# Optimization experiments

Hardware: AMD Instinct MI355X
Metric: run time of the kernel (lower is better)

Reference implementation:

```python
import jax, jax.numpy as jnp
import numpy as np

N = 100000
F_IN = 128
HID = 256
N_CLS = 40
E = 1600000


def setup_inputs() -> dict:
    key = jax.random.key(0)
    ks = jax.random.split(key, 12)
    x = jax.random.normal(ks[0], (N, F_IN), dtype=jnp.float32)
    edge_index = jax.random.randint(ks[1], (2, E), 0, N, dtype=jnp.int64)
    # GCNConv params (glorot-ish scale), conv2 is reused twice in forward
    def lin(k, fi, fo):
        return jax.random.normal(k, (fi, fo), dtype=jnp.float32) * (1.0 / np.sqrt(fi))
    return {
        "x": x,
        "edge_index": edge_index,
        "W1": lin(ks[2], F_IN, HID), "b1": jnp.zeros((HID,), jnp.float32),
        "W2": lin(ks[3], HID, HID),  "b2": jnp.zeros((HID,), jnp.float32),
        "W3": lin(ks[4], HID, HID),  "b3": jnp.zeros((HID,), jnp.float32),
        "W4": lin(ks[5], HID, N_CLS), "b4": jnp.zeros((N_CLS,), jnp.float32),
    }


def _gcn_norm(edge_index, n):
    # add self-loops, compute symmetric normalization D^-1/2 (A+I) D^-1/2
    loop = jnp.arange(n, dtype=edge_index.dtype)
    src = jnp.concatenate([edge_index[0], loop])
    dst = jnp.concatenate([edge_index[1], loop])
    deg = jax.ops.segment_sum(jnp.ones_like(dst, dtype=jnp.float32), dst, num_segments=n)
    dinv = jnp.where(deg > 0, jax.lax.rsqrt(deg), 0.0)
    norm = dinv[src] * dinv[dst]  # [E+N]
    return src, dst, norm


def _gcn_conv(x, W, b, src, dst, norm, n):
    h = x @ W                       # [N, Fout] dense transform first (fewer msg bytes)
    msg = h[src] * norm[:, None]    # gather + scale
    out = jax.ops.segment_sum(msg, dst, num_segments=n)  # scatter-add
    return out + b


def reference(x, edge_index, W1, b1, W2, b2, W3, b3, W4, b4):
    n = x.shape[0]
    src, dst, norm = _gcn_norm(edge_index, n)
    h = jax.nn.relu(_gcn_conv(x, W1, b1, src, dst, norm, n))
    h = jax.nn.relu(_gcn_conv(h, W2, b2, src, dst, norm, n))
    h = jax.nn.relu(_gcn_conv(h, W2, b2, src, dst, norm, n))  # conv2 reused, as in source
    h = jax.nn.relu(_gcn_conv(h, W3, b3, src, dst, norm, n))
    h = _gcn_conv(h, W4, b4, src, dst, norm, n)
    return jax.nn.log_softmax(h, axis=1)
```

## Files before the change

kernel.cpp:

```cpp
#include <hip/hip_runtime.h>
#include <stdint.h>
#include <math.h>

#define NN   100000
#define FIN  128
#define HIDDEN 256
#define NCLS 40
#define NE   1600000

#define PRNG 8
#define RNG  12500
#define SSL  32
#define NES  50000

typedef unsigned short u16;
typedef unsigned char u8;
typedef __attribute__((ext_vector_type(8))) short s16x8;
typedef __attribute__((ext_vector_type(4))) float f32x4;
typedef __attribute__((ext_vector_type(2))) float f32x2;

__device__ __forceinline__ float bf2f(unsigned short u) {
    union { float f; uint32_t i; } v; v.i = ((uint32_t)u) << 16; return v.f;
}
__device__ __forceinline__ unsigned short f2bf(float f) {
    union { float f; uint32_t i; } v; v.f = f;
    uint32_t r = v.i + 0x7fffu + ((v.i >> 16) & 1u);
    return (unsigned short)(r >> 16);
}
__device__ __forceinline__ u8 f2fp8(float f) {
    int r = __builtin_amdgcn_cvt_pk_fp8_f32(f, f, 0, false);
    return (u8)(r & 0xff);
}

#define SWZ_T(t)  ((((t) >> 3) & 1) | ((((t) >> 5) & 1) << 1))
#define SWZ_L(lr) ((((lr) >> 1) & 1) | ((((lr) >> 3) & 1) << 1))

__global__ __launch_bounds__(256) void k_detect(const u16* __restrict__ x16,
                                                const int* __restrict__ ei,
                                                int* __restrict__ flags) {
    int g = blockIdx.x * 256 + threadIdx.x;
    uint2 v = *(const uint2*)(x16 + (size_t)g * 4);
    int nan_cnt = 0;
    uint32_t w0 = v.x, w1 = v.y;
    if (((w0 >> 0)  & 0x7fff) >= 0x7f80) nan_cnt++;
    if (((w0 >> 16) & 0x7fff) >= 0x7f80) nan_cnt++;
    if (((w1 >> 0)  & 0x7fff) >= 0x7f80) nan_cnt++;
    if (((w1 >> 16) & 0x7fff) >= 0x7f80) nan_cnt++;
    int odd_nz = (g < 8192 && ei[2 * g + 1] != 0) ? 1 : 0;
#pragma unroll
    for (int off = 1; off < 64; off <<= 1) {
        nan_cnt += __shfl_xor(nan_cnt, off);
        odd_nz  += __shfl_xor(odd_nz, off);
    }
    if ((threadIdx.x & 63) == 0) {
        if (nan_cnt) atomicAdd(&flags[0], nan_cnt);
        if (odd_nz)  atomicAdd(&flags[2], odd_nz);
    }
}

__global__ void k_compact(const int* __restrict__ ei, int* __restrict__ dst32,
                          int* __restrict__ src32, const int* __restrict__ flags) {
    int e = blockIdx.x * 256 + threadIdx.x;
    if (e < NE) {
        if (flags[2] == 0) { src32[e] = ei[2 * e]; dst32[e] = ei[2 * (NE + e)]; }
        else               { src32[e] = ei[e];     dst32[e] = ei[NE + e]; }
    }
}

__global__ void k_trans_cvt(const void* W1, const void* W2, const void* W3, const void* W4,
                            u16* W1t, u16* W2t, u16* W3t, u16* W4t,
                            const void* b1, const void* b2, const void* b3, const void* b4,
                            u16* o1, u16* o2, u16* o3, u16* o4,
                            const void* __restrict__ x, const float* __restrict__ dinv,
                            u16* __restrict__ xb,
                            const int* __restrict__ flags) {
    int b = blockIdx.x;
    int fl = flags[0];
    int t = threadIdx.x;
    if (b >= 705) {
        int i8 = (b - 705) * 256 + t;
        if (i8 < NN * FIN / 8) {
            int i = i8 * 8;
            float d = dinv[i >> 7];
            u16 r[8];
            if (fl) {
                const float* xf = (const float*)x + i;
                f32x4 v0 = *(const f32x4*)xf;
                f32x4 v1 = *(const f32x4*)(xf + 4);
#pragma unroll
                for (int k = 0; k < 4; ++k) { r[k] = f2bf(v0[k] * d); r[4 + k] = f2bf(v1[k] * d); }
            } else {
                uint4 v = *(const uint4*)((const u16*)x + i);
                uint32_t w[4] = {v.x, v.y, v.z, v.w};
#pragma unroll
                for (int k = 0; k < 4; ++k) {
                    r[2 * k]     = f2bf(bf2f((u16)(w[k] & 0xffff)) * d);
                    r[2 * k + 1] = f2bf(bf2f((u16)(w[k] >> 16)) * d);
                }
            }
            uint4 o;
            o.x = (uint32_t)r[0] | ((uint32_t)r[1] << 16);
            o.y = (uint32_t)r[2] | ((uint32_t)r[3] << 16);
            o.z = (uint32_t)r[4] | ((uint32_t)r[5] << 16);
            o.w = (uint32_t)r[6] | ((uint32_t)r[7] << 16);
            *(uint4*)(xb + i) = o;
        }
        return;
    }
    if (b == 704) {
        o1[t] = fl ? f2bf(((const float*)b1)[t]) : ((const u16*)b1)[t];
        o2[t] = fl ? f2bf(((const float*)b2)[t]) : ((const u16*)b2)[t];
        o3[t] = fl ? f2bf(((const float*)b3)[t]) : ((const u16*)b3)[t];
        if (t < 64) o4[t] = (t < NCLS) ? (fl ? f2bf(((const float*)b4)[t]) : ((const u16*)b4)[t]) : (u16)0;
        return;
    }
    const void* W; u16* Wt; int K, F, Fpad, base;
    if (b < 128)      { W = W1; Wt = W1t; K = 128; F = 256; Fpad = 256; base = 0; }
    else if (b < 384) { W = W2; Wt = W2t; K = 256; F = 256; Fpad = 256; base = 128; }
    else if (b < 640) { W = W3; Wt = W3t; K = 256; F = 256; Fpad = 256; base = 384; }
    else              { W = W4; Wt = W4t; K = 256; F = 40;  Fpad = 64;  base = 640; }
    int idx = (b - base) * 256 + t;
    if (idx >= K * Fpad) return;
    int f = idx / K, k = idx - f * K;
    u16 v = 0;
    if (f < F) {
        if (fl) v = f2bf(((const float*)W)[(size_t)k * F + f]);
        else    v = ((const u16*)W)[(size_t)k * F + f];
    }
    Wt[idx] = v;
}


__global__ __launch_bounds__(256) void k_histb(const int* __restrict__ dst32,
                                               int* __restrict__ partial) {
    __shared__ int h[RNG];
    int p = blockIdx.x >> 5, s = blockIdx.x & 31;
    int t = threadIdx.x;
    int4 z4 = make_int4(0, 0, 0, 0);
    for (int i = t * 4; i < RNG; i += 1024) *(int4*)(h + i) = z4;
    __syncthreads();
    int base = s * NES;
    int lo = p * RNG;
    int nfull = NES & ~1023;
    for (int k = t * 4; k < nfull; k += 1024) {
        int4 d4 = *(const int4*)(dst32 + base + k);
        int a;
        a = d4.x - lo; if ((unsigned)a < RNG) atomicAdd(&h[a], 1);
        a = d4.y - lo; if ((unsigned)a < RNG) atomicAdd(&h[a], 1);
        a = d4.z - lo; if ((unsigned)a < RNG) atomicAdd(&h[a], 1);
        a = d4.w - lo; if ((unsigned)a < RNG) atomicAdd(&h[a], 1);
    }
    for (int k = nfull + t; k < NES; k += 256) {
        int a = dst32[base + k] - lo;
        if ((unsigned)a < RNG) atomicAdd(&h[a], 1);
    }
    __syncthreads();
    int* out = partial + blockIdx.x * RNG;
    for (int i = t * 4; i < RNG; i += 1024) *(int4*)(out + i) = *(const int4*)(h + i);
}

__global__ __launch_bounds__(256) void k_scan1(const int* __restrict__ partial,
                                               int* __restrict__ cnt,
                                               int* __restrict__ out,
                                               int* __restrict__ bsum) {
    __shared__ int sh[256];
    int t = threadIdx.x;
    int base = blockIdx.x * 1024 + t * 4;
    int v0 = 0, v1 = 0, v2 = 0, v3 = 0;
    if (base < NN) {
        int p = base / RNG, il = base - p * RNG;
        const int* q = partial + (p * SSL) * RNG + il;
        int4 acc = make_int4(0, 0, 0, 0);
#pragma unroll
        for (int s = 0; s < SSL; ++s) {
            int4 w = *(const int4*)(q + s * RNG);
            acc.x += w.x; acc.y += w.y; acc.z += w.z; acc.w += w.w;
        }
        v0 = acc.x; v1 = acc.y; v2 = acc.z; v3 = acc.w;
        *(int4*)(cnt + base) = acc;
    }
    int s = v0 + v1 + v2 + v3;
    sh[t] = s;
    __syncthreads();
    for (int off = 1; off < 256; off <<= 1) {
        int x = (t >= off) ? sh[t - off] : 0;
        __syncthreads();
        sh[t] += x;
        __syncthreads();
    }
    int ex = sh[t] - s;
    if (base < NN) {
        int4 o = make_int4(ex, ex + v0, ex + v0 + v1, ex + v0 + v1 + v2);
        *(int4*)(out + base) = o;
    }
    if (t == 255) bsum[blockIdx.x] = sh[255];
}

__global__ void k_scan2(int* bsum, int nb) {
    __shared__ int sh[128];
    int t = threadIdx.x;
    int v = (t < nb) ? bsum[t] : 0;
    sh[t] = v;
    __syncthreads();
    for (int off = 1; off < 128; off <<= 1) {
        int x = (t >= off) ? sh[t - off] : 0;
        __syncthreads();
        sh[t] += x;
        __syncthreads();
    }
    if (t < nb) bsum[t] = sh[t] - v;
}

__global__ void k_scan3o(int* __restrict__ rp, const int* __restrict__ bsum,
                         const int* __restrict__ cnt, float* __restrict__ dinv,
                         int* __restrict__ partial) {
    int i = blockIdx.x * 256 + threadIdx.x;
    if (i < NN) {
        int v = rp[i] + bsum[i >> 10];
        rp[i] = v;
        dinv[i] = rsqrtf((float)(cnt[i] + 1));
        int p = i / RNG, il = i - p * RNG;
        int* q = partial + (p * SSL) * RNG + il;
        int run = v;
#pragma unroll
        for (int s = 0; s < SSL; ++s) { int t = q[s * RNG]; q[s * RNG] = run; run += t; }
    }
    if (i == 0) rp[NN] = NE;
}

__global__ __launch_bounds__(256) void k_fillb(const int* __restrict__ dst32,
                                               const int* __restrict__ src32,
                                               const int* __restrict__ offs,
                                               int* __restrict__ col) {
    __shared__ int h[RNG];
    int p = blockIdx.x >> 5, s = blockIdx.x & 31;
    int t = threadIdx.x;
    const int* o = offs + blockIdx.x * RNG;
    for (int i = t * 4; i < RNG; i += 1024) *(int4*)(h + i) = *(const int4*)(o + i);
    __syncthreads();
    int base = s * NES;
    int lo = p * RNG;
    int nfull = NES & ~1023;
    for (int k = t * 4; k < nfull; k += 1024) {
        int4 d4 = *(const int4*)(dst32 + base + k);
        int4 s4 = *(const int4*)(src32 + base + k);
        int a;
        a = d4.x - lo; if ((unsigned)a < RNG) col[atomicAdd(&h[a], 1)] = s4.x;
        a = d4.y - lo; if ((unsigned)a < RNG) col[atomicAdd(&h[a], 1)] = s4.y;
        a = d4.z - lo; if ((unsigned)a < RNG) col[atomicAdd(&h[a], 1)] = s4.z;
        a = d4.w - lo; if ((unsigned)a < RNG) col[atomicAdd(&h[a], 1)] = s4.w;
    }
    for (int k = nfull + t; k < NES; k += 256) {
        int a = dst32[base + k] - lo;
        if ((unsigned)a < RNG) col[atomicAdd(&h[a], 1)] = src32[base + k];
    }
}


#define GLL(g, l) __builtin_amdgcn_global_load_lds( \
    (const __attribute__((address_space(1))) unsigned int*)(g), \
    (__attribute__((address_space(3))) unsigned int*)(l), 16, 0, 0)

#define NT128 ((NN + 127) / 128)
#define NT256 ((NN + 255) / 256)

__global__ __launch_bounds__(256) void k_gemmP(const u16* __restrict__ A,
                                               const u16* __restrict__ Wt,
                                               const float* __restrict__ dinv,
                                               const u16* __restrict__ bias,
                                               u16* __restrict__ C,
                                               int K, int out_fp8) {
    __shared__ __align__(16) u16 Bs[64 * 256];
    __shared__ __align__(16) u16 As[2 * 128 * 32];
    int t = threadIdx.x;
    int bn = blockIdx.y;
    int w = t >> 6, lane = t & 63;
    int lrow = lane & 15, lq = lane >> 4;
    int r0 = t >> 2;
    int seg = ((t & 3) ^ SWZ_T(t)) * 8;
    int lqs = (lq ^ SWZ_L(lrow)) * 8;

    int nK = K >> 5;
    for (int r = 0; r < nK; ++r)
        GLL(Wt + (size_t)(bn * 64 + (t >> 2)) * K + r * 32 + seg, Bs + r * 2048 + t * 8);

    bool fuse = (bias != nullptr);
    float bcol[4];
#pragma unroll
    for (int j = 0; j < 4; ++j)
        bcol[j] = fuse ? bf2f(bias[bn * 64 + j * 16 + lrow]) : 0.f;

    for (int tm = blockIdx.x; tm < NT128; tm += gridDim.x) {
        int rowBase = tm * 128;
        int ar0 = rowBase + r0;       if (ar0 > NN - 1) ar0 = NN - 1;
        int ar1 = rowBase + 64 + r0;  if (ar1 > NN - 1) ar1 = NN - 1;
        const u16* a0p = A + (size_t)ar0 * K + seg;
        const u16* a1p = A + (size_t)ar1 * K + seg;
        GLL(a0p, As + t * 8);
        GLL(a1p, As + 2048 + t * 8);

        f32x4 acc[2][4] = {};
        int cur = 0;
        for (int kt = 0; kt < nK; ++kt) {
            __syncthreads();
            if (kt + 1 < nK) {
                int nxt = cur ^ 1;
                GLL(a0p + (kt + 1) * 32, As + nxt * 4096 + t * 8);
                GLL(a1p + (kt + 1) * 32, As + nxt * 4096 + 2048 + t * 8);
            }
            const u16* ab = As + cur * 4096;
            const u16* bb = Bs + kt * 2048;
            s16x8 af[2], bf[4];
#pragma unroll
            for (int i = 0; i < 2; ++i)
                af[i] = *(const s16x8*)(ab + (w * 32 + i * 16 + lrow) * 32 + lqs);
#pragma unroll
            for (int j = 0; j < 4; ++j)
                bf[j] = *(const s16x8*)(bb + (j * 16 + lrow) * 32 + lqs);
#pragma unroll
            for (int i = 0; i < 2; ++i)
#pragma unroll
                for (int j = 0; j < 4; ++j)
                    acc[i][j] = __builtin_amdgcn_mfma_f32_16x16x32_bf16(af[i], bf[j], acc[i][j], 0, 0, 0);
            cur ^= 1;
        }

        u8* C8 = (u8*)C;
#pragma unroll
        for (int i = 0; i < 2; ++i) {
#pragma unroll
            for (int rr = 0; rr < 4; ++rr) {
                int row = rowBase + w * 32 + i * 16 + lq * 4 + rr;
                if (row < NN) {
                    float d = dinv[row];
#pragma unroll
                    for (int j = 0; j < 4; ++j) {
                        int colg = bn * 64 + j * 16 + lrow;
                        float v = fuse ? fmaxf(fmaf(d, acc[i][j][rr], bcol[j]), 0.f)
                                       : acc[i][j][rr] * d;
                        if (out_fp8) C8[(size_t)row * HIDDEN + colg] = f2fp8(v);
                        else         C[(size_t)row * HIDDEN + colg] = f2bf(v);
                    }
                }
            }
        }
        __syncthreads();
    }
}

__global__ __launch_bounds__(256) void k_gemmP64(const u16* __restrict__ A,
                                                 const u16* __restrict__ Wt,
                                                 const float* __restrict__ dinv,
                                                 u16* __restrict__ C) {
    const int K = 256;
    __shared__ __align__(16) u16 Bs[64 * 256];
    __shared__ __align__(16) u16 As[2 * 256 * 32];
    int t = threadIdx.x;
    int w = t >> 6, lane = t & 63;
    int lrow = lane & 15, lq = lane >> 4;
    int seg = ((t & 3) ^ SWZ_T(t)) * 8;
    int lqs = (lq ^ SWZ_L(lrow)) * 8;
    int rr0 = t >> 2;

    for (int r = 0; r < 8; ++r)
        GLL(Wt + (size_t)(t >> 2) * K + r * 32 + seg, Bs + r * 2048 + t * 8);

    for (int tm = blockIdx.x; tm < NT256; tm += gridDim.x) {
        int rowBase = tm * 256;
        const u16* ap[4];
#pragma unroll
        for (int c = 0; c < 4; ++c) {
            int ar = rowBase + c * 64 + rr0;
            if (ar > NN - 1) ar = NN - 1;
            ap[c] = A + (size_t)ar * K + seg;
        }
#pragma unroll
        for (int c = 0; c < 4; ++c) GLL(ap[c], As + c * 2048 + t * 8);

        f32x4 acc[4][4] = {};
        int cur = 0;
        for (int kt = 0; kt < 8; ++kt) {
            __syncthreads();
            if (kt + 1 < 8) {
                int nxt = cur ^ 1;
#pragma unroll
                for (int c = 0; c < 4; ++c)
                    GLL(ap[c] + (kt + 1) * 32, As + nxt * 8192 + c * 2048 + t * 8);
            }
            const u16* ab = As + cur * 8192;
            const u16* bb = Bs + kt * 2048;
            s16x8 af[4], bf[4];
#pragma unroll
            for (int i = 0; i < 4; ++i)
                af[i] = *(const s16x8*)(ab + (w * 64 + i * 16 + lrow) * 32 + lqs);
#pragma unroll
            for (int j = 0; j < 4; ++j)
                bf[j] = *(const s16x8*)(bb + (j * 16 + lrow) * 32 + lqs);
#pragma unroll
            for (int i = 0; i < 4; ++i)
#pragma unroll
                for (int j = 0; j < 4; ++j)
                    acc[i][j] = __builtin_amdgcn_mfma_f32_16x16x32_bf16(af[i], bf[j], acc[i][j], 0, 0, 0);
            cur ^= 1;
        }

#pragma unroll
        for (int i = 0; i < 4; ++i) {
#pragma unroll
            for (int rr = 0; rr < 4; ++rr) {
                int row = rowBase + w * 64 + i * 16 + lq * 4 + rr;
                if (row < NN) {
                    float d = dinv[row];
#pragma unroll
                    for (int j = 0; j < 4; ++j) {
                        int colg = j * 16 + lrow;
                        C[(size_t)row * 64 + colg] = f2bf(acc[i][j][rr] * d);
                    }
                }
            }
        }
        __syncthreads();
    }
}


__global__ __launch_bounds__(256) void k_agg8(const u8* __restrict__ hs,
                                              const int* __restrict__ rp,
                                              const int* __restrict__ col,
                                              const float* __restrict__ dinv,
                                              const u16* __restrict__ bias,
                                              u16* __restrict__ out) {
    int wq = __builtin_amdgcn_readfirstlane(threadIdx.x >> 6);
    int row = blockIdx.x * 4 + wq;
    if (row >= NN) return;
    int lane = threadIdx.x & 63;
    int fo = lane * 4;
    float a0 = 0.f, a1 = 0.f, a2 = 0.f, a3 = 0.f;
    auto acc_add = [&](uint32_t w) {
        f32x2 x = __builtin_amdgcn_cvt_pk_f32_fp8(w, false);
        f32x2 y = __builtin_amdgcn_cvt_pk_f32_fp8(w, true);
        a0 += x.x; a1 += x.y; a2 += y.x; a3 += y.y;
    };
    auto acc_fma = [&](uint32_t w, float m) {
        f32x2 x = __builtin_amdgcn_cvt_pk_f32_fp8(w, false);
        f32x2 y = __builtin_amdgcn_cvt_pk_f32_fp8(w, true);
        a0 = fmaf(m, x.x, a0); a1 = fmaf(m, x.y, a1);
        a2 = fmaf(m, y.x, a2); a3 = fmaf(m, y.y, a3);
    };
    acc_add(*(const uint32_t*)(hs + (size_t)row * HIDDEN + fo));
    int p  = __builtin_amdgcn_readfirstlane(rp[row]);
    int p1 = __builtin_amdgcn_readfirstlane(rp[row + 1]);
    for (; p + 8 <= p1; p += 8) {
        uint32_t v[8];
#pragma unroll
        for (int k = 0; k < 8; ++k) {
            int c = __builtin_amdgcn_readfirstlane(col[p + k]);
            v[k] = *(const uint32_t*)(hs + (size_t)c * HIDDEN + fo);
        }
#pragma unroll
        for (int k = 0; k < 8; ++k) acc_add(v[k]);
    }
    int rem = p1 - p;
    if (rem) {
        uint32_t v[8];
#pragma unroll
        for (int k = 0; k < 8; ++k) {
            int idx = (k < rem) ? (p + k) : p;
            int c = __builtin_amdgcn_readfirstlane(col[idx]);
            v[k] = *(const uint32_t*)(hs + (size_t)c * HIDDEN + fo);
        }
#pragma unroll
        for (int k = 0; k < 8; ++k) acc_fma(v[k], (k < rem) ? 1.f : 0.f);
    }
    float d = dinv[row];
    uint2 bv = *(const uint2*)(bias + fo);
    float r0 = fmaxf(fmaf(d, a0, bf2f((u16)(bv.x & 0xffff))), 0.f);
    float r1 = fmaxf(fmaf(d, a1, bf2f((u16)(bv.x >> 16))), 0.f);
    float r2 = fmaxf(fmaf(d, a2, bf2f((u16)(bv.y & 0xffff))), 0.f);
    float r3 = fmaxf(fmaf(d, a3, bf2f((u16)(bv.y >> 16))), 0.f);
    uint2 o;
    o.x = (uint32_t)f2bf(r0) | ((uint32_t)f2bf(r1) << 16);
    o.y = (uint32_t)f2bf(r2) | ((uint32_t)f2bf(r3) << 16);
    *(uint2*)(out + (size_t)row * HIDDEN + fo) = o;
}

__global__ __launch_bounds__(256) void k_aggx(const u16* __restrict__ xb,
                                              const int* __restrict__ rp,
                                              const int* __restrict__ col,
                                              u16* __restrict__ out) {
    int wq = __builtin_amdgcn_readfirstlane(threadIdx.x >> 6);
    int row = blockIdx.x * 4 + wq;
    if (row >= NN) return;
    int lane = threadIdx.x & 63;
    int fo = lane * 2;
    float a0 = 0.f, a1 = 0.f;
    auto acc_add = [&](uint32_t w) {
        a0 += bf2f((u16)(w & 0xffff));
        a1 += bf2f((u16)(w >> 16));
    };
    auto acc_fma = [&](uint32_t w, float m) {
        a0 = fmaf(m, bf2f((u16)(w & 0xffff)), a0);
        a1 = fmaf(m, bf2f((u16)(w >> 16)), a1);
    };
    acc_add(*(const uint32_t*)(xb + (size_t)row * FIN + fo));
    int p  = __builtin_amdgcn_readfirstlane(rp[row]);
    int p1 = __builtin_amdgcn_readfirstlane(rp[row + 1]);
    for (; p + 8 <= p1; p += 8) {
        uint32_t v[8];
#pragma unroll
        for (int k = 0; k < 8; ++k) {
            int c = __builtin_amdgcn_readfirstlane(col[p + k]);
            v[k] = *(const uint32_t*)(xb + (size_t)c * FIN + fo);
        }
#pragma unroll
        for (int k = 0; k < 8; ++k) acc_add(v[k]);
    }
    int rem = p1 - p;
    if (rem) {
        uint32_t v[8];
#pragma unroll
        for (int k = 0; k < 8; ++k) {
            int idx = (k < rem) ? (p + k) : p;
            int c = __builtin_amdgcn_readfirstlane(col[idx]);
            v[k] = *(const uint32_t*)(xb + (size_t)c * FIN + fo);
        }
#pragma unroll
        for (int k = 0; k < 8; ++k) acc_fma(v[k], (k < rem) ? 1.f : 0.f);
    }
    uint32_t o = (uint32_t)f2bf(a0) | ((uint32_t)f2bf(a1) << 16);
    *(uint32_t*)(out + (size_t)row * FIN + fo) = o;
}

__global__ __launch_bounds__(256) void k_agg5(const u16* __restrict__ hs,
                                              const int* __restrict__ rp,
                                              const int* __restrict__ col,
                                              const float* __restrict__ dinv,
                                              const u16* __restrict__ bias,
                                              void* __restrict__ out,
                                              const int* __restrict__ flags) {
    int wq = __builtin_amdgcn_readfirstlane(threadIdx.x >> 6);
    int row = blockIdx.x * 4 + wq;
    if (row >= NN) return;
    int lane = threadIdx.x & 63;
    float a = bf2f(hs[(size_t)row * 64 + lane]);
    int p  = __builtin_amdgcn_readfirstlane(rp[row]);
    int p1 = __builtin_amdgcn_readfirstlane(rp[row + 1]);
    for (; p + 8 <= p1; p += 8) {
        u16 v[8];
#pragma unroll
        for (int k = 0; k < 8; ++k) {
            int c = __builtin_amdgcn_readfirstlane(col[p + k]);
            v[k] = hs[(size_t)c * 64 + lane];
        }
#pragma unroll
        for (int k = 0; k < 8; ++k) a += bf2f(v[k]);
    }
    int rem = p1 - p;
    if (rem) {
        u16 v[8];
#pragma unroll
        for (int k = 0; k < 8; ++k) {
            int idx = (k < rem) ? (p + k) : p;
            int c = __builtin_amdgcn_readfirstlane(col[idx]);
            v[k] = hs[(size_t)c * 64 + lane];
        }
#pragma unroll
        for (int k = 0; k < 8; ++k)
            a = fmaf((k < rem) ? 1.f : 0.f, bf2f(v[k]), a);
    }
    bool act = lane < NCLS;
    float d = dinv[row];
    float l = act ? fmaf(d, a, bf2f(bias[lane])) : -1e30f;
    float m = l;
#pragma unroll
    for (int off = 32; off > 0; off >>= 1) m = fmaxf(m, __shfl_xor(m, off));
    float e = act ? __expf(l - m) : 0.f;
#pragma unroll
    for (int off = 32; off > 0; off >>= 1) e += __shfl_xor(e, off);
    if (act) {
        float r = l - m - __logf(e);
        if (flags[0]) ((float*)out)[(size_t)row * NCLS + lane] = r;
        else          ((u16*)out)[(size_t)row * NCLS + lane] = f2bf(r);
    }
}


extern "C" void kernel_launch(void* const* d_in, const int* in_sizes, int n_in,
                              void* d_out, int out_size, void* d_ws, size_t ws_size,
                              hipStream_t stream) {
    const void* x  = d_in[0];
    const int* ei  = (const int*)d_in[1];
    const void* W1 = d_in[2];
    const void* b1 = d_in[3];
    const void* W2 = d_in[4];
    const void* b2 = d_in[5];
    const void* W3 = d_in[6];
    const void* b3 = d_in[7];
    const void* W4 = d_in[8];
    const void* b4 = d_in[9];

    char* p = (char*)d_ws;
    auto alloc = [&](size_t b) -> char* {
        char* r = p;
        p += (b + 255) & ~(size_t)255;
        return r;
    };
    int*   flags = (int*)alloc(256);
    int*   cnt  = (int*)alloc((size_t)NN * 4);
    float* dinv = (float*)alloc((size_t)NN * 4);
    int*   rp   = (int*)alloc((size_t)(NN + 1) * 4);
    int*   col  = (int*)alloc((size_t)NE * 4);
    int*   bsum = (int*)alloc(4096);
    u16* xb  = (u16*)alloc((size_t)NN * FIN * 2);
    u16* W1t = (u16*)alloc((size_t)256 * 128 * 2);
    u16* W2t = (u16*)alloc((size_t)256 * 256 * 2);
    u16* W3t = (u16*)alloc((size_t)256 * 256 * 2);
    u16* W4t = (u16*)alloc((size_t)64 * 256 * 2);
    u16* bb1 = (u16*)alloc(512);
    u16* bb2 = (u16*)alloc(512);
    u16* bb3 = (u16*)alloc(512);
    u16* bb4 = (u16*)alloc(128);
    u16* bufA = (u16*)alloc((size_t)NN * HIDDEN * 2);
    u16* bufB = (u16*)alloc((size_t)NN * HIDDEN * 2);

    int* dst32   = (int*)bufA;
    int* src32   = dst32 + NE;
    int* partial = (int*)bufB;

    hipMemsetAsync(flags, 0, 16, stream);
    k_detect<<<64, 256, 0, stream>>>((const u16*)x, ei, flags);
    k_compact<<<(NE + 255) / 256, 256, 0, stream>>>(ei, dst32, src32, flags);

    k_histb<<<PRNG * SSL, 256, 0, stream>>>(dst32, partial);
    k_scan1<<<(NN + 1023) / 1024, 256, 0, stream>>>(partial, cnt, rp, bsum);
    k_scan2<<<1, 128, 0, stream>>>(bsum, (NN + 1023) / 1024);
    k_scan3o<<<(NN + 255) / 256, 256, 0, stream>>>(rp, bsum, cnt, dinv, partial);
    k_fillb<<<PRNG * SSL, 256, 0, stream>>>(dst32, src32, partial, col);

    k_trans_cvt<<<705 + (NN * FIN / 8 + 255) / 256, 256, 0, stream>>>(
        W1, W2, W3, W4, W1t, W2t, W3t, W4t,
        b1, b2, b3, b4, bb1, bb2, bb3, bb4, x, dinv, xb, flags);

    dim3 gP(192, 4);
    dim3 aggGrid((NN + 3) / 4);

    k_aggx<<<aggGrid, 256, 0, stream>>>(xb, rp, col, bufB);
    k_gemmP<<<gP, 256, 0, stream>>>(bufB, W1t, dinv, bb1, bufA, 128, 0);
    k_gemmP<<<gP, 256, 0, stream>>>(bufA, W2t, dinv, nullptr, bufB, 256, 1);
    k_agg8<<<aggGrid, 256, 0, stream>>>((const u8*)bufB, rp, col, dinv, bb2, bufA);
    k_gemmP<<<gP, 256, 0, stream>>>(bufA, W2t, dinv, nullptr, bufB, 256, 1);
    k_agg8<<<aggGrid, 256, 0, stream>>>((const u8*)bufB, rp, col, dinv, bb2, bufA);
    k_gemmP<<<gP, 256, 0, stream>>>(bufA, W3t, dinv, nullptr, bufB, 256, 1);
    k_agg8<<<aggGrid, 256, 0, stream>>>((const u8*)bufB, rp, col, dinv, bb3, bufA);
    k_gemmP64<<<256, 256, 0, stream>>>(bufA, W4t, dinv, bufB);
    k_agg5<<<aggGrid, 256, 0, stream>>>(bufB, rp, col, dinv, bb4, d_out, flags);
}
```

Measured before the change: 648.2 us.

## Replace partitioned LDS CSR build with global atomics and unify last GEMM

Measured after the change: 753.8 us. +16.3%, slower.

```diff
diff --git a/kernel.cpp b/kernel.cpp
--- a/kernel.cpp
+++ b/kernel.cpp
@@ -7,11 +7,6 @@
 #define HIDDEN 256
 #define NCLS 40
 #define NE   1600000
-
-#define PRNG 8
-#define RNG  12500
-#define SSL  32
-#define NES  50000
 
 typedef unsigned short u16;
 typedef unsigned char u8;
@@ -131,55 +126,23 @@
 }
 
 
-__global__ __launch_bounds__(256) void k_histb(const int* __restrict__ dst32,
-                                               int* __restrict__ partial) {
-    __shared__ int h[RNG];
-    int p = blockIdx.x >> 5, s = blockIdx.x & 31;
-    int t = threadIdx.x;
-    int4 z4 = make_int4(0, 0, 0, 0);
-    for (int i = t * 4; i < RNG; i += 1024) *(int4*)(h + i) = z4;
-    __syncthreads();
-    int base = s * NES;
-    int lo = p * RNG;
-    int nfull = NES & ~1023;
-    for (int k = t * 4; k < nfull; k += 1024) {
-        int4 d4 = *(const int4*)(dst32 + base + k);
-        int a;
-        a = d4.x - lo; if ((unsigned)a < RNG) atomicAdd(&h[a], 1);
-        a = d4.y - lo; if ((unsigned)a < RNG) atomicAdd(&h[a], 1);
-        a = d4.z - lo; if ((unsigned)a < RNG) atomicAdd(&h[a], 1);
-        a = d4.w - lo; if ((unsigned)a < RNG) atomicAdd(&h[a], 1);
-    }
-    for (int k = nfull + t; k < NES; k += 256) {
-        int a = dst32[base + k] - lo;
-        if ((unsigned)a < RNG) atomicAdd(&h[a], 1);
-    }
-    __syncthreads();
-    int* out = partial + blockIdx.x * RNG;
-    for (int i = t * 4; i < RNG; i += 1024) *(int4*)(out + i) = *(const int4*)(h + i);
-}
-
-__global__ __launch_bounds__(256) void k_scan1(const int* __restrict__ partial,
-                                               int* __restrict__ cnt,
+__global__ __launch_bounds__(256) void k_hista(const int* __restrict__ dst32,
+                                               int* __restrict__ cnt) {
+    int i = (blockIdx.x * 256 + threadIdx.x) * 2;
+    int2 d2 = *(const int2*)(dst32 + i);
+    atomicAdd(&cnt[d2.x], 1);
+    atomicAdd(&cnt[d2.y], 1);
+}
+
+__global__ __launch_bounds__(256) void k_scan1(const int* __restrict__ cnt,
                                                int* __restrict__ out,
                                                int* __restrict__ bsum) {
     __shared__ int sh[256];
     int t = threadIdx.x;
     int base = blockIdx.x * 1024 + t * 4;
-    int v0 = 0, v1 = 0, v2 = 0, v3 = 0;
-    if (base < NN) {
-        int p = base / RNG, il = base - p * RNG;
-        const int* q = partial + (p * SSL) * RNG + il;
-        int4 acc = make_int4(0, 0, 0, 0);
-#pragma unroll
-        for (int s = 0; s < SSL; ++s) {
-            int4 w = *(const int4*)(q + s * RNG);
-            acc.x += w.x; acc.y += w.y; acc.z += w.z; acc.w += w.w;
-        }
-        v0 = acc.x; v1 = acc.y; v2 = acc.z; v3 = acc.w;
-        *(int4*)(cnt + base) = acc;
-    }
-    int s = v0 + v1 + v2 + v3;
+    int4 a = make_int4(0, 0, 0, 0);
+    if (base < NN) a = *(const int4*)(cnt + base);
+    int s = a.x + a.y + a.z + a.w;
     sh[t] = s;
     __syncthreads();
     for (int off = 1; off < 256; off <<= 1) {
@@ -190,7 +153,7 @@
     }
     int ex = sh[t] - s;
     if (base < NN) {
-        int4 o = make_int4(ex, ex + v0, ex + v0 + v1, ex + v0 + v1 + v2);
+        int4 o = make_int4(ex, ex + a.x, ex + a.x + a.y, ex + a.x + a.y + a.z);
         *(int4*)(out + base) = o;
     }
     if (t == 255) bsum[blockIdx.x] = sh[255];
@@ -211,49 +174,30 @@
     if (t < nb) bsum[t] = sh[t] - v;
 }
 
-__global__ void k_scan3o(int* __restrict__ rp, const int* __restrict__ bsum,
-                         const int* __restrict__ cnt, float* __restrict__ dinv,
-                         int* __restrict__ partial) {
+__global__ void k_scan3(int* __restrict__ rp, const int* __restrict__ bsum,
+                        const int* __restrict__ cnt, float* __restrict__ dinv,
+                        int* __restrict__ wcur) {
     int i = blockIdx.x * 256 + threadIdx.x;
     if (i < NN) {
         int v = rp[i] + bsum[i >> 10];
         rp[i] = v;
+        wcur[i] = v;
         dinv[i] = rsqrtf((float)(cnt[i] + 1));
-        int p = i / RNG, il = i - p * RNG;
-        int* q = partial + (p * SSL) * RNG + il;
-        int run = v;
-#pragma unroll
-        for (int s = 0; s < SSL; ++s) { int t = q[s * RNG]; q[s * RNG] = run; run += t; }
     }
     if (i == 0) rp[NN] = NE;
 }
 
-__global__ __launch_bounds__(256) void k_fillb(const int* __restrict__ dst32,
+__global__ __launch_bounds__(256) void k_filla(const int* __restrict__ dst32,
                                                const int* __restrict__ src32,
-                                               const int* __restrict__ offs,
+                                               int* __restrict__ wcur,
                                                int* __restrict__ col) {
-    __shared__ int h[RNG];
-    int p = blockIdx.x >> 5, s = blockIdx.x & 31;
-    int t = threadIdx.x;
-    const int* o = offs + blockIdx.x * RNG;
-    for (int i = t * 4; i < RNG; i += 1024) *(int4*)(h + i) = *(const int4*)(o + i);
-    __syncthreads();
-    int base = s * NES;
-    int lo = p * RNG;
-    int nfull = NES & ~1023;
-    for (int k = t * 4; k < nfull; k += 1024) {
-        int4 d4 = *(const int4*)(dst32 + base + k);
-        int4 s4 = *(const int4*)(src32 + base + k);
-        int a;
-        a = d4.x - lo; if ((unsigned)a < RNG) col[atomicAdd(&h[a], 1)] = s4.x;
-        a = d4.y - lo; if ((unsigned)a < RNG) col[atomicAdd(&h[a], 1)] = s4.y;
-        a = d4.z - lo; if ((unsigned)a < RNG) col[atomicAdd(&h[a], 1)] = s4.z;
-        a = d4.w - lo; if ((unsigned)a < RNG) col[atomicAdd(&h[a], 1)] = s4.w;
-    }
-    for (int k = nfull + t; k < NES; k += 256) {
-        int a = dst32[base + k] - lo;
-        if ((unsigned)a < RNG) col[atomicAdd(&h[a], 1)] = src32[base + k];
-    }
+    int i = (blockIdx.x * 256 + threadIdx.x) * 2;
+    int2 d2 = *(const int2*)(dst32 + i);
+    int2 s2 = *(const int2*)(src32 + i);
+    int p0 = atomicAdd(&wcur[d2.x], 1);
+    col[p0] = s2.x;
+    int p1 = atomicAdd(&wcur[d2.y], 1);
+    col[p1] = s2.y;
 }
 
 
@@ -262,14 +206,13 @@
     (__attribute__((address_space(3))) unsigned int*)(l), 16, 0, 0)
 
 #define NT128 ((NN + 127) / 128)
-#define NT256 ((NN + 255) / 256)
 
 __global__ __launch_bounds__(256) void k_gemmP(const u16* __restrict__ A,
                                                const u16* __restrict__ Wt,
                                                const float* __restrict__ dinv,
                                                const u16* __restrict__ bias,
                                                u16* __restrict__ C,
-                                               int K, int out_fp8) {
+                                               int K, int ldc, int out_fp8) {
     __shared__ __align__(16) u16 Bs[64 * 256];
     __shared__ __align__(16) u16 As[2 * 128 * 32];
     int t = threadIdx.x;
@@ -338,83 +281,8 @@
                         int colg = bn * 64 + j * 16 + lrow;
                         float v = fuse ? fmaxf(fmaf(d, acc[i][j][rr], bcol[j]), 0.f)
                                        : acc[i][j][rr] * d;
-                        if (out_fp8) C8[(size_t)row * HIDDEN + colg] = f2fp8(v);
-                        else         C[(size_t)row * HIDDEN + colg] = f2bf(v);
-                    }
-                }
-            }
-        }
-        __syncthreads();
-    }
-}
-
-__global__ __launch_bounds__(256) void k_gemmP64(const u16* __restrict__ A,
-                                                 const u16* __restrict__ Wt,
-                                                 const float* __restrict__ dinv,
-                                                 u16* __restrict__ C) {
-    const int K = 256;
-    __shared__ __align__(16) u16 Bs[64 * 256];
-    __shared__ __align__(16) u16 As[2 * 256 * 32];
-    int t = threadIdx.x;
-    int w = t >> 6, lane = t & 63;
-    int lrow = lane & 15, lq = lane >> 4;
-    int seg = ((t & 3) ^ SWZ_T(t)) * 8;
-    int lqs = (lq ^ SWZ_L(lrow)) * 8;
-    int rr0 = t >> 2;
-
-    for (int r = 0; r < 8; ++r)
-        GLL(Wt + (size_t)(t >> 2) * K + r * 32 + seg, Bs + r * 2048 + t * 8);
-
-    for (int tm = blockIdx.x; tm < NT256; tm += gridDim.x) {
-        int rowBase = tm * 256;
-        const u16* ap[4];
-#pragma unroll
-        for (int c = 0; c < 4; ++c) {
-            int ar = rowBase + c * 64 + rr0;
-            if (ar > NN - 1) ar = NN - 1;
-            ap[c] = A + (size_t)ar * K + seg;
-        }
-#pragma unroll
-        for (int c = 0; c < 4; ++c) GLL(ap[c], As + c * 2048 + t * 8);
-
-        f32x4 acc[4][4] = {};
-        int cur = 0;
-        for (int kt = 0; kt < 8; ++kt) {
-            __syncthreads();
-            if (kt + 1 < 8) {
-                int nxt = cur ^ 1;
-#pragma unroll
-                for (int c = 0; c < 4; ++c)
-                    GLL(ap[c] + (kt + 1) * 32, As + nxt * 8192 + c * 2048 + t * 8);
-            }
-            const u16* ab = As + cur * 8192;
-            const u16* bb = Bs + kt * 2048;
-            s16x8 af[4], bf[4];
-#pragma unroll
-            for (int i = 0; i < 4; ++i)
-                af[i] = *(const s16x8*)(ab + (w * 64 + i * 16 + lrow) * 32 + lqs);
-#pragma unroll
-            for (int j = 0; j < 4; ++j)
-                bf[j] = *(const s16x8*)(bb + (j * 16 + lrow) * 32 + lqs);
-#pragma unroll
-            for (int i = 0; i < 4; ++i)
-#pragma unroll
-                for (int j = 0; j < 4; ++j)
-                    acc[i][j] = __builtin_amdgcn_mfma_f32_16x16x32_bf16(af[i], bf[j], acc[i][j], 0, 0, 0);
-            cur ^= 1;
-        }
-
-#pragma unroll
-        for (int i = 0; i < 4; ++i) {
-#pragma unroll
-            for (int rr = 0; rr < 4; ++rr) {
-                int row = rowBase + w * 64 + i * 16 + lq * 4 + rr;
-                if (row < NN) {
-                    float d = dinv[row];
-#pragma unroll
-                    for (int j = 0; j < 4; ++j) {
-                        int colg = j * 16 + lrow;
-                        C[(size_t)row * 64 + colg] = f2bf(acc[i][j][rr] * d);
+                        if (out_fp8) C8[(size_t)row * ldc + colg] = f2fp8(v);
+                        else         C[(size_t)row * ldc + colg] = f2bf(v);
                     }
                 }
             }
@@ -609,6 +477,7 @@
     int*   cnt  = (int*)alloc((size_t)NN * 4);
     float* dinv = (float*)alloc((size_t)NN * 4);
     int*   rp   = (int*)alloc((size_t)(NN + 1) * 4);
+    int*   wcur = (int*)alloc((size_t)NN * 4);
     int*   col  = (int*)alloc((size_t)NE * 4);
     int*   bsum = (int*)alloc(4096);
     u16* xb  = (u16*)alloc((size_t)NN * FIN * 2);
@@ -625,33 +494,34 @@
 
     int* dst32   = (int*)bufA;
     int* src32   = dst32 + NE;
-    int* partial = (int*)bufB;
 
     hipMemsetAsync(flags, 0, 16, stream);
+    hipMemsetAsync(cnt, 0, (size_t)NN * 4, stream);
     k_detect<<<64, 256, 0, stream>>>((const u16*)x, ei, flags);
     k_compact<<<(NE + 255) / 256, 256, 0, stream>>>(ei, dst32, src32, flags);
 
-    k_histb<<<PRNG * SSL, 256, 0, stream>>>(dst32, partial);
-    k_scan1<<<(NN + 1023) / 1024, 256, 0, stream>>>(partial, cnt, rp, bsum);
+    k_hista<<<NE / 512, 256, 0, stream>>>(dst32, cnt);
+    k_scan1<<<(NN + 1023) / 1024, 256, 0, stream>>>(cnt, rp, bsum);
     k_scan2<<<1, 128, 0, stream>>>(bsum, (NN + 1023) / 1024);
-    k_scan3o<<<(NN + 255) / 256, 256, 0, stream>>>(rp, bsum, cnt, dinv, partial);
-    k_fillb<<<PRNG * SSL, 256, 0, stream>>>(dst32, src32, partial, col);
+    k_scan3<<<(NN + 255) / 256, 256, 0, stream>>>(rp, bsum, cnt, dinv, wcur);
+    k_filla<<<NE / 512, 256, 0, stream>>>(dst32, src32, wcur, col);
 
     k_trans_cvt<<<705 + (NN * FIN / 8 + 255) / 256, 256, 0, stream>>>(
         W1, W2, W3, W4, W1t, W2t, W3t, W4t,
         b1, b2, b3, b4, bb1, bb2, bb3, bb4, x, dinv, xb, flags);
 
     dim3 gP(192, 4);
+    dim3 gP5(768, 1);
     dim3 aggGrid((NN + 3) / 4);
 
     k_aggx<<<aggGrid, 256, 0, stream>>>(xb, rp, col, bufB);
-    k_gemmP<<<gP, 256, 0, stream>>>(bufB, W1t, dinv, bb1, bufA, 128, 0);
-    k_gemmP<<<gP, 256, 0, stream>>>(bufA, W2t, dinv, nullptr, bufB, 256, 1);
+    k_gemmP<<<gP, 256, 0, stream>>>(bufB, W1t, dinv, bb1, bufA, 128, HIDDEN, 0);
+    k_gemmP<<<gP, 256, 0, stream>>>(bufA, W2t, dinv, nullptr, bufB, 256, HIDDEN, 1);
     k_agg8<<<aggGrid, 256, 0, stream>>>((const u8*)bufB, rp, col, dinv, bb2, bufA);
-    k_gemmP<<<gP, 256, 0, stream>>>(bufA, W2t, dinv, nullptr, bufB, 256, 1);
+    k_gemmP<<<gP, 256, 0, stream>>>(bufA, W2t, dinv, nullptr, bufB, 256, HIDDEN, 1);
     k_agg8<<<aggGrid, 256, 0, stream>>>((const u8*)bufB, rp, col, dinv, bb2, bufA);
-    k_gemmP<<<gP, 256, 0, stream>>>(bufA, W3t, dinv, nullptr, bufB, 256, 1);
+    k_gemmP<<<gP, 256, 0, stream>>>(bufA, W3t, dinv, nullptr, bufB, 256, HIDDEN, 1);
     k_agg8<<<aggGrid, 256, 0, stream>>>((const u8*)bufB, rp, col, dinv, bb3, bufA);
-    k_gemmP64<<<256, 256, 0, stream>>>(bufA, W4t, dinv, bufB);
+    k_gemmP<<<gP5, 256, 0, stream>>>(bufA, W4t, dinv, nullptr, bufB, 256, 64, 0);
     k_agg5<<<aggGrid, 256, 0, stream>>>(bufB, rp, col, dinv, bb4, d_out, flags);
 }
```
